# Performance work log

Measured on AMD Instinct MI355X. Metric: run time of the kernel, lower is better.

## Reference

```python
import jax, jax.numpy as jnp
import numpy as np


def setup_inputs() -> dict:
    key = jax.random.key(0)
    k1, k2, k3, k4, k5 = jax.random.split(key, 5)
    B, H, S, D = 2, 8, 256, 64
    return {
        "query": jax.random.normal(k1, (B, H, S, D), dtype=jnp.float32),
        "key": jax.random.normal(k2, (B, H, S, D), dtype=jnp.float32),
        "val": jax.random.normal(k3, (B, H, S, D), dtype=jnp.float32),
        "key_structure": jax.random.normal(k4, (B, H, S, S, D), dtype=jnp.float32),
        "val_structure": jax.random.normal(k5, (B, H, S, S, D), dtype=jnp.float32),
        "attention_mask": jnp.ones((B, S), dtype=jnp.float32),
    }


def reference(query, key, val, key_structure, val_structure, attention_mask):
    d_k = query.shape[-1]
    # QK^T scores: [B,H,Sq,Sk]
    scores = jnp.einsum("bhqd,bhkd->bhqk", query, key)
    # additive edge-structure bias: per-(q,k) key embedding dotted with query
    scores = scores + jnp.einsum("bhqd,bhqkd->bhqk", query, key_structure)
    # faithful to original: mask [B,S] -> [B,1,S,1] (masks along query axis), added BEFORE scaling
    mask = (1.0 - attention_mask)[:, None, :, None] * -100000.0
    scores = (scores + mask) / np.float32(d_k ** 0.5)
    attn = jax.nn.softmax(scores, axis=-1)
    out = jnp.einsum("bhqk,bhkd->bhqd", attn, val)
    out = out + jnp.einsum("bhqk,bhqkd->bhqd", attn, val_structure)
    return out, attn
```

## Files before the change

kernel.cpp:

```cpp
#include <hip/hip_runtime.h>
#include <math.h>

#define BB 2
#define HH 8
#define SS 256
#define DD 64

__global__ __launch_bounds__(256) void attn_struct_kernel(
    const float* __restrict__ query,
    const float* __restrict__ key,
    const float* __restrict__ val,
    const float* __restrict__ kst,
    const float* __restrict__ vst,
    const float* __restrict__ amask,
    float* __restrict__ out,
    float* __restrict__ attn_out)
{
    const int tid  = threadIdx.x;
    const int lane = tid & 63;
    const int warp = tid >> 6;
    const int blk  = blockIdx.x;
    const int q_idx = blk & (SS - 1);
    const int bh    = blk >> 8;
    const int b     = bh >> 3;

    const float* qptr  = query + (size_t)blk * DD;
    const float* kbase = key   + (size_t)bh  * SS * DD;
    const float* vbase = val   + (size_t)bh  * SS * DD;
    const float* kstp  = kst   + (size_t)blk * SS * DD;
    const float* vstp  = vst   + (size_t)blk * SS * DD;

    __shared__ float sc[SS];
    __shared__ float redm[4];
    __shared__ float reds[4];
    __shared__ float redo[4][DD];

    const int kr = tid >> 4;
    const int dg = tid & 15;

    const float4 qv = *(const float4*)(qptr + dg * 4);

    #pragma unroll 4
    for (int it = 0; it < 16; ++it) {
        const int k = it * 16 + kr;
        const float4 kv = *(const float4*)(kbase + (size_t)k * DD + dg * 4);
        const float4 sv = *(const float4*)(kstp  + (size_t)k * DD + dg * 4);
        float p = qv.x * (kv.x + sv.x) + qv.y * (kv.y + sv.y)
                + qv.z * (kv.z + sv.z) + qv.w * (kv.w + sv.w);
        p += __shfl_xor(p, 1);
        p += __shfl_xor(p, 2);
        p += __shfl_xor(p, 4);
        p += __shfl_xor(p, 8);
        if (dg == 0) sc[k] = p;
    }
    __syncthreads();

    const float maskv = (1.0f - amask[b * SS + q_idx]) * -100000.0f;
    float s = (sc[tid] + maskv) * 0.125f;

    float m = s;
    m = fmaxf(m, __shfl_xor(m, 1));
    m = fmaxf(m, __shfl_xor(m, 2));
    m = fmaxf(m, __shfl_xor(m, 4));
    m = fmaxf(m, __shfl_xor(m, 8));
    m = fmaxf(m, __shfl_xor(m, 16));
    m = fmaxf(m, __shfl_xor(m, 32));
    if (lane == 0) redm[warp] = m;
    __syncthreads();
    m = fmaxf(fmaxf(redm[0], redm[1]), fmaxf(redm[2], redm[3]));

    const float e = __expf(s - m);
    float t = e;
    t += __shfl_xor(t, 1);
    t += __shfl_xor(t, 2);
    t += __shfl_xor(t, 4);
    t += __shfl_xor(t, 8);
    t += __shfl_xor(t, 16);
    t += __shfl_xor(t, 32);
    if (lane == 0) reds[warp] = t;
    __syncthreads();
    const float tot = reds[0] + reds[1] + reds[2] + reds[3];
    const float a = e / tot;

    attn_out[(size_t)blk * SS + tid] = a;
    __syncthreads();
    sc[tid] = a;
    __syncthreads();

    float4 acc = make_float4(0.f, 0.f, 0.f, 0.f);
    #pragma unroll 4
    for (int it = 0; it < 16; ++it) {
        const int k = it * 16 + kr;
        const float aw = sc[k];
        const float4 vv = *(const float4*)(vbase + (size_t)k * DD + dg * 4);
        const float4 sv = *(const float4*)(vstp  + (size_t)k * DD + dg * 4);
        acc.x += aw * (vv.x + sv.x);
        acc.y += aw * (vv.y + sv.y);
        acc.z += aw * (vv.z + sv.z);
        acc.w += aw * (vv.w + sv.w);
    }
    acc.x += __shfl_xor(acc.x, 16); acc.y += __shfl_xor(acc.y, 16);
    acc.z += __shfl_xor(acc.z, 16); acc.w += __shfl_xor(acc.w, 16);
    acc.x += __shfl_xor(acc.x, 32); acc.y += __shfl_xor(acc.y, 32);
    acc.z += __shfl_xor(acc.z, 32); acc.w += __shfl_xor(acc.w, 32);
    if (lane < 16) {
        redo[warp][lane * 4 + 0] = acc.x;
        redo[warp][lane * 4 + 1] = acc.y;
        redo[warp][lane * 4 + 2] = acc.z;
        redo[warp][lane * 4 + 3] = acc.w;
    }
    __syncthreads();
    if (tid < DD) {
        out[(size_t)blk * DD + tid] =
            redo[0][tid] + redo[1][tid] + redo[2][tid] + redo[3][tid];
    }
}

extern "C" void kernel_launch(void* const* d_in, const int* in_sizes, int n_in,
                              void* d_out, int out_size, void* d_ws, size_t ws_size,
                              hipStream_t stream) {
    const float* query = (const float*)d_in[0];
    const float* key   = (const float*)d_in[1];
    const float* val   = (const float*)d_in[2];
    const float* kst   = (const float*)d_in[3];
    const float* vst   = (const float*)d_in[4];
    const float* amask = (const float*)d_in[5];

    float* out  = (float*)d_out;
    float* attn = out + (size_t)BB * HH * SS * DD;

    attn_struct_kernel<<<BB * HH * SS, 256, 0, stream>>>(
        query, key, val, kst, vst, amask, out, attn);
}
```

Before: 512.6 us.

## Fully unroll score loop, reduce partials via padded LDS, use nontemporal structure loads

The score loop is fully unrolled so all 16 key/structure loads can be in flight, and the per-row shuffle reductions are replaced by writing partial dot products to a padded shared buffer that each thread then sums for its own key. The streamed key/value structure tensors are read with nontemporal loads to avoid polluting caches, and a redundant barrier is removed. Launch bounds now request 4 blocks per CU. The extra ~17KB of LDS and the higher register use from full unrolling may limit occupancy.

```diff
diff --git a/kernel.cpp b/kernel.cpp
--- a/kernel.cpp
+++ b/kernel.cpp
@@ -5,8 +5,11 @@
 #define HH 8
 #define SS 256
 #define DD 64
+#define PAD 17
 
-__global__ __launch_bounds__(256) void attn_struct_kernel(
+typedef float vfloat4 __attribute__((ext_vector_type(4)));
+
+__global__ __launch_bounds__(256, 4) void attn_struct_kernel(
     const float* __restrict__ query,
     const float* __restrict__ key,
     const float* __restrict__ val,
@@ -30,6 +33,7 @@
     const float* kstp  = kst   + (size_t)blk * SS * DD;
     const float* vstp  = vst   + (size_t)blk * SS * DD;
 
+    __shared__ float part[SS * PAD];
     __shared__ float sc[SS];
     __shared__ float redm[4];
     __shared__ float reds[4];
@@ -38,25 +42,30 @@
     const int kr = tid >> 4;
     const int dg = tid & 15;
 
-    const float4 qv = *(const float4*)(qptr + dg * 4);
+    const vfloat4 qv = *(const vfloat4*)(qptr + dg * 4);
 
-    #pragma unroll 4
+    float p[16];
+    #pragma unroll
     for (int it = 0; it < 16; ++it) {
         const int k = it * 16 + kr;
-        const float4 kv = *(const float4*)(kbase + (size_t)k * DD + dg * 4);
-        const float4 sv = *(const float4*)(kstp  + (size_t)k * DD + dg * 4);
-        float p = qv.x * (kv.x + sv.x) + qv.y * (kv.y + sv.y)
-                + qv.z * (kv.z + sv.z) + qv.w * (kv.w + sv.w);
-        p += __shfl_xor(p, 1);
-        p += __shfl_xor(p, 2);
-        p += __shfl_xor(p, 4);
-        p += __shfl_xor(p, 8);
-        if (dg == 0) sc[k] = p;
+        const vfloat4 kv = *(const vfloat4*)(kbase + (size_t)k * DD + dg * 4);
+        const vfloat4 sv = __builtin_nontemporal_load(
+            (const vfloat4*)(kstp + (size_t)k * DD + dg * 4));
+        p[it] = qv.x * (kv.x + sv.x) + qv.y * (kv.y + sv.y)
+              + qv.z * (kv.z + sv.z) + qv.w * (kv.w + sv.w);
+    }
+    #pragma unroll
+    for (int it = 0; it < 16; ++it) {
+        part[(it * 16 + kr) * PAD + dg] = p[it];
     }
     __syncthreads();
 
+    float s = 0.f;
+    #pragma unroll
+    for (int j = 0; j < 16; ++j) s += part[tid * PAD + j];
+
     const float maskv = (1.0f - amask[b * SS + q_idx]) * -100000.0f;
-    float s = (sc[tid] + maskv) * 0.125f;
+    s = (s + maskv) * 0.125f;
 
     float m = s;
     m = fmaxf(m, __shfl_xor(m, 1));
@@ -83,17 +92,17 @@
     const float a = e / tot;
 
     attn_out[(size_t)blk * SS + tid] = a;
-    __syncthreads();
     sc[tid] = a;
     __syncthreads();
 
-    float4 acc = make_float4(0.f, 0.f, 0.f, 0.f);
-    #pragma unroll 4
+    vfloat4 acc = (vfloat4)(0.f);
+    #pragma unroll
     for (int it = 0; it < 16; ++it) {
         const int k = it * 16 + kr;
         const float aw = sc[k];
-        const float4 vv = *(const float4*)(vbase + (size_t)k * DD + dg * 4);
-        const float4 sv = *(const float4*)(vstp  + (size_t)k * DD + dg * 4);
+        const vfloat4 vv = *(const vfloat4*)(vbase + (size_t)k * DD + dg * 4);
+        const vfloat4 sv = __builtin_nontemporal_load(
+            (const vfloat4*)(vstp + (size_t)k * DD + dg * 4));
         acc.x += aw * (vv.x + sv.x);
         acc.y += aw * (vv.y + sv.y);
         acc.z += aw * (vv.z + sv.z);
```

Measured after the change: 499.4 us. 2.6% less time.
